# Optimization experiments

Measured on AMD Instinct MI355X. Metric: run time of the kernel, lower is better.

## Reference

```python
import jax, jax.numpy as jnp
import numpy as np

B, S, H = 64, 2048, 256
H3 = 3 * H


def setup_inputs() -> dict:
    key = jax.random.key(0)
    ks = jax.random.split(key, 5)
    static = jax.random.normal(ks[0], (B, S, H), dtype=jnp.float32)
    dynamic = jax.random.normal(ks[1], (B, S, H), dtype=jnp.float32)
    decoder_hidden = jax.random.normal(ks[2], (B, H), dtype=jnp.float32)
    # learned params (nn.Parameter in original); scale ~ 1/sqrt(fan_in)
    v = jax.random.normal(ks[3], (1, H3), dtype=jnp.float32) / np.sqrt(H3)
    W = jax.random.normal(ks[4], (H3, H3), dtype=jnp.float32) / np.sqrt(H3)
    return {"static": static, "dynamic": dynamic,
            "decoder_hidden": decoder_hidden, "v": v, "W": W}


def reference(static, dynamic, decoder_hidden, v, W):
    # cat = concat(static[i,j], dynamic[i,j], decoder_hidden[i]) -> [B, S, 3H]
    dec = jnp.broadcast_to(decoder_hidden[:, None, :], static.shape)
    cat = jnp.concatenate([static, dynamic, dec], axis=-1)
    # score[b,s] = v . tanh(W @ cat[b,s])
    hidden = jnp.tanh(jnp.einsum('ok,bsk->bso', W, cat))  # [B, S, 3H]
    scores = jnp.einsum('bso,o->bs', hidden, v[0])        # [B, S]
    return jax.nn.softmax(scores, axis=1)
```

## Files before the change

### kernel.cpp

```cpp
#include <hip/hip_runtime.h>
#include <hip/hip_bf16.h>

#define B_   64
#define S_   2048
#define H_   256
#define H3_  768
#define K_   512
#define MT   64

typedef __attribute__((ext_vector_type(8))) short  bf16x8;
typedef __attribute__((ext_vector_type(4))) float  f32x4;

__device__ __forceinline__ ushort f2bf(float f) {
    __hip_bfloat16 h = __float2bfloat16(f);
    return *reinterpret_cast<ushort*>(&h);
}

__device__ __forceinline__ float fast_tanh(float x) {
    float e = __expf(2.0f * x);
    return 1.0f - 2.0f / (e + 1.0f);
}

__global__ void pack_w(const float* __restrict__ W, short* __restrict__ wpk) {
    int t = blockIdx.x * 256 + threadIdx.x;
    if (t >= 48 * 16 * 64) return;
    int lane = t & 63;
    int ks   = (t >> 6) & 15;
    int ot   = t >> 10;
    int o  = ot * 16 + (lane & 15);
    int kb = ks * 32 + (lane >> 4) * 8;
    const float* src = W + (size_t)o * H3_ + kb;
    float4 a = ((const float4*)src)[0];
    float4 b = ((const float4*)src)[1];
    union { bf16x8 v; uint4 u; } pk;
    pk.u.x = (uint)f2bf(a.x) | ((uint)f2bf(a.y) << 16);
    pk.u.y = (uint)f2bf(a.z) | ((uint)f2bf(a.w) << 16);
    pk.u.z = (uint)f2bf(b.x) | ((uint)f2bf(b.y) << 16);
    pk.u.w = (uint)f2bf(b.z) | ((uint)f2bf(b.w) << 16);
    *(bf16x8*)(wpk + (size_t)t * 8) = pk.v;
}

__global__ void bias_k(const float* __restrict__ W, const float* __restrict__ dec,
                       float* __restrict__ bias) {
    int idx = blockIdx.x * 256 + threadIdx.x;
    if (idx >= B_ * H3_) return;
    int b = idx / H3_;
    int o = idx - b * H3_;
    const float4* wr = (const float4*)(W + (size_t)o * H3_ + 2 * H_);
    const float4* dv = (const float4*)(dec + (size_t)b * H_);
    float s = 0.f;
#pragma unroll 8
    for (int k = 0; k < H_ / 4; ++k) {
        float4 a = wr[k], d = dv[k];
        s += a.x * d.x + a.y * d.y + a.z * d.z + a.w * d.w;
    }
    bias[idx] = s;
}

__global__ __launch_bounds__(256, 2)
void score_k(const float* __restrict__ stat, const float* __restrict__ dyn,
             const short* __restrict__ wpk, const float* __restrict__ bias,
             const float* __restrict__ v, float* __restrict__ scores) {
    __shared__ short aT[MT * K_];
    __shared__ float sred[4][MT];

    const int tid  = threadIdx.x;
    const int pos0 = blockIdx.x * MT;
    const int bidx = pos0 >> 11;

#pragma unroll
    for (int bat = 0; bat < 2; ++bat) {
        float4 f0[8], f1[8];
#pragma unroll
        for (int u = 0; u < 8; ++u) {
            int lin = (bat * 8 + u) * 256 + tid;
            int row = lin >> 6;
            int k   = (lin & 63) * 8;
            const float* src = (k < 256)
                ? (stat + (size_t)(pos0 + row) * H_ + k)
                : (dyn  + (size_t)(pos0 + row) * H_ + (k - 256));
            f0[u] = ((const float4*)src)[0];
            f1[u] = ((const float4*)src)[1];
        }
#pragma unroll
        for (int u = 0; u < 8; ++u) {
            int lin = (bat * 8 + u) * 256 + tid;
            int row = lin >> 6;
            int k   = (lin & 63) * 8;
            uint4 pk;
            pk.x = (uint)f2bf(f0[u].x) | ((uint)f2bf(f0[u].y) << 16);
            pk.y = (uint)f2bf(f0[u].z) | ((uint)f2bf(f0[u].w) << 16);
            pk.z = (uint)f2bf(f1[u].x) | ((uint)f2bf(f1[u].y) << 16);
            pk.w = (uint)f2bf(f1[u].z) | ((uint)f2bf(f1[u].w) << 16);
            int off = row * (K_ * 2) + k * 2;
            off ^= (row & 7) << 4;
            *(uint4*)((char*)aT + off) = pk;
        }
    }
    __syncthreads();

    const int wave = tid >> 6;
    const int lane = tid & 63;
    const int lr = lane & 15;
    const int lg = lane >> 4;

    float sacc[4][4];
#pragma unroll
    for (int mi = 0; mi < 4; ++mi)
#pragma unroll
        for (int j = 0; j < 4; ++j) sacc[mi][j] = 0.f;

    for (int pass = 0; pass < 3; ++pass) {
        const int obase = pass * 256 + wave * 64;
        f32x4 acc[4][4];
#pragma unroll
        for (int mi = 0; mi < 4; ++mi)
#pragma unroll
            for (int ni = 0; ni < 4; ++ni) acc[mi][ni] = (f32x4)0.f;

#pragma unroll 4
        for (int ks = 0; ks < 16; ++ks) {
            bf16x8 bfr[4];
#pragma unroll
            for (int ni = 0; ni < 4; ++ni) {
                int ot = pass * 16 + wave * 4 + ni;
                bfr[ni] = *(const bf16x8*)(wpk +
                    ((size_t)(ot * 16 + ks) * 64 + lane) * 8);
            }
            const int kb = ks * 32 + lg * 8;
            bf16x8 afr[4];
#pragma unroll
            for (int mi = 0; mi < 4; ++mi) {
                int row = mi * 16 + lr;
                int off = row * (K_ * 2) + kb * 2;
                off ^= (row & 7) << 4;
                afr[mi] = *(const bf16x8*)((const char*)aT + off);
            }
#pragma unroll
            for (int mi = 0; mi < 4; ++mi)
#pragma unroll
                for (int ni = 0; ni < 4; ++ni)
                    acc[mi][ni] = __builtin_amdgcn_mfma_f32_16x16x32_bf16(
                        afr[mi], bfr[ni], acc[mi][ni], 0, 0, 0);
        }

#pragma unroll
        for (int ni = 0; ni < 4; ++ni) {
            int o = obase + ni * 16 + lr;
            float bv = bias[bidx * H3_ + o];
            float vv = v[o];
#pragma unroll
            for (int mi = 0; mi < 4; ++mi)
#pragma unroll
                for (int j = 0; j < 4; ++j)
                    sacc[mi][j] += vv * fast_tanh(acc[mi][ni][j] + bv);
        }
    }

#pragma unroll
    for (int mi = 0; mi < 4; ++mi)
#pragma unroll
        for (int j = 0; j < 4; ++j) {
            float x = sacc[mi][j];
            x += __shfl_xor(x, 1);
            x += __shfl_xor(x, 2);
            x += __shfl_xor(x, 4);
            x += __shfl_xor(x, 8);
            sacc[mi][j] = x;
        }
    if (lr == 0) {
#pragma unroll
        for (int mi = 0; mi < 4; ++mi)
#pragma unroll
            for (int j = 0; j < 4; ++j)
                sred[wave][mi * 16 + lg * 4 + j] = sacc[mi][j];
    }
    __syncthreads();
    if (tid < MT) {
        float s = sred[0][tid] + sred[1][tid] + sred[2][tid] + sred[3][tid];
        scores[pos0 + tid] = s;
    }
}

__global__ void softmax_k(float* __restrict__ out) {
    const int b = blockIdx.x;
    float* row = out + (size_t)b * S_;
    const int tid  = threadIdx.x;
    const int wave = tid >> 6;
    const int lane = tid & 63;

    float vals[8];
    float m = -1e30f;
#pragma unroll
    for (int i = 0; i < 8; ++i) {
        vals[i] = row[tid + i * 256];
        m = fmaxf(m, vals[i]);
    }
#pragma unroll
    for (int off = 32; off >= 1; off >>= 1) m = fmaxf(m, __shfl_xor(m, off));
    __shared__ float redm[4];
    __shared__ float reds[4];
    if (lane == 0) redm[wave] = m;
    __syncthreads();
    m = fmaxf(fmaxf(redm[0], redm[1]), fmaxf(redm[2], redm[3]));

    float s = 0.f;
#pragma unroll
    for (int i = 0; i < 8; ++i) {
        vals[i] = __expf(vals[i] - m);
        s += vals[i];
    }
#pragma unroll
    for (int off = 32; off >= 1; off >>= 1) s += __shfl_xor(s, off);
    if (lane == 0) reds[wave] = s;
    __syncthreads();
    s = reds[0] + reds[1] + reds[2] + reds[3];
    float inv = 1.0f / s;
#pragma unroll
    for (int i = 0; i < 8; ++i) row[tid + i * 256] = vals[i] * inv;
}

extern "C" void kernel_launch(void* const* d_in, const int* in_sizes, int n_in,
                              void* d_out, int out_size, void* d_ws, size_t ws_size,
                              hipStream_t stream) {
    const float* stat = (const float*)d_in[0];
    const float* dyn  = (const float*)d_in[1];
    const float* dec  = (const float*)d_in[2];
    const float* v    = (const float*)d_in[3];
    const float* W    = (const float*)d_in[4];
    float* out = (float*)d_out;

    short* wpk  = (short*)d_ws;
    float* bias = (float*)((char*)d_ws + (size_t)H3_ * K_ * 2);

    pack_w <<<(48 * 16 * 64 + 255) / 256, 256, 0, stream>>>(W, wpk);
    bias_k <<<(B_ * H3_ + 255) / 256, 256, 0, stream>>>(W, dec, bias);
    score_k<<<(B_ * S_) / MT, 256, 0, stream>>>(stat, dyn, wpk, bias, v, out);
    softmax_k<<<B_, 256, 0, stream>>>(out);
}
```

Before: 162.9 us.

## Double the row tile to 128 with 8 waves and pipeline K-chunk staging

The score kernel now handles 128 positions per block with 512 threads, and each wave owns a 96-column slice of the output so the W fragments are reused across 8 row tiles. The activation tile is staged in four K-quarters. The global loads for the next quarter are issued while MFMAs run on the current quarter, overlapping HBM latency with compute instead of loading everything up front. The trade-off is higher register pressure (8x3 accumulators plus prefetch buffers) and 128KB of LDS per block, which may limit occupancy to one block per CU.

```diff
diff --git a/kernel.cpp b/kernel.cpp
--- a/kernel.cpp
+++ b/kernel.cpp
@@ -6,7 +6,7 @@
 #define H_   256
 #define H3_  768
 #define K_   512
-#define MT   64
+#define MT   128
 
 typedef __attribute__((ext_vector_type(8))) short  bf16x8;
 typedef __attribute__((ext_vector_type(4))) float  f32x4;
@@ -57,46 +57,50 @@
     bias[idx] = s;
 }
 
-__global__ __launch_bounds__(256, 2)
+__global__ __launch_bounds__(512, 2)
 void score_k(const float* __restrict__ stat, const float* __restrict__ dyn,
              const short* __restrict__ wpk, const float* __restrict__ bias,
              const float* __restrict__ v, float* __restrict__ scores) {
-    __shared__ short aT[MT * K_];
-    __shared__ float sred[4][MT];
+    __shared__ short aT[4 * MT * 128];
+    __shared__ float sred[8][MT];
 
     const int tid  = threadIdx.x;
     const int pos0 = blockIdx.x * MT;
     const int bidx = pos0 >> 11;
 
-#pragma unroll
-    for (int bat = 0; bat < 2; ++bat) {
-        float4 f0[8], f1[8];
-#pragma unroll
-        for (int u = 0; u < 8; ++u) {
-            int lin = (bat * 8 + u) * 256 + tid;
-            int row = lin >> 6;
-            int k   = (lin & 63) * 8;
-            const float* src = (k < 256)
-                ? (stat + (size_t)(pos0 + row) * H_ + k)
-                : (dyn  + (size_t)(pos0 + row) * H_ + (k - 256));
+    float4 f0[4], f1[4];
+    auto stage_load = [&](int q) {
+#pragma unroll
+        for (int u = 0; u < 4; ++u) {
+            int lin = u * 512 + tid;
+            int row = lin >> 4;
+            int kl  = (lin & 15) * 8;
+            const float* src = (q < 2)
+                ? (stat + (size_t)(pos0 + row) * H_ + q * 128 + kl)
+                : (dyn  + (size_t)(pos0 + row) * H_ + (q - 2) * 128 + kl);
             f0[u] = ((const float4*)src)[0];
             f1[u] = ((const float4*)src)[1];
         }
-#pragma unroll
-        for (int u = 0; u < 8; ++u) {
-            int lin = (bat * 8 + u) * 256 + tid;
-            int row = lin >> 6;
-            int k   = (lin & 63) * 8;
+    };
+    auto stage_write = [&](int q) {
+#pragma unroll
+        for (int u = 0; u < 4; ++u) {
+            int lin = u * 512 + tid;
+            int row = lin >> 4;
+            int kl  = (lin & 15) * 8;
             uint4 pk;
             pk.x = (uint)f2bf(f0[u].x) | ((uint)f2bf(f0[u].y) << 16);
             pk.y = (uint)f2bf(f0[u].z) | ((uint)f2bf(f0[u].w) << 16);
             pk.z = (uint)f2bf(f1[u].x) | ((uint)f2bf(f1[u].y) << 16);
             pk.w = (uint)f2bf(f1[u].z) | ((uint)f2bf(f1[u].w) << 16);
-            int off = row * (K_ * 2) + k * 2;
+            int off = q * 32768 + row * 256 + kl * 2;
             off ^= (row & 7) << 4;
             *(uint4*)((char*)aT + off) = pk;
         }
-    }
+    };
+
+    stage_load(0);
+    stage_write(0);
     __syncthreads();
 
     const int wave = tid >> 6;
@@ -104,53 +108,58 @@
     const int lr = lane & 15;
     const int lg = lane >> 4;
 
-    float sacc[4][4];
-#pragma unroll
-    for (int mi = 0; mi < 4; ++mi)
+    float sacc[8][4];
+#pragma unroll
+    for (int mi = 0; mi < 8; ++mi)
 #pragma unroll
         for (int j = 0; j < 4; ++j) sacc[mi][j] = 0.f;
 
-    for (int pass = 0; pass < 3; ++pass) {
-        const int obase = pass * 256 + wave * 64;
-        f32x4 acc[4][4];
-#pragma unroll
-        for (int mi = 0; mi < 4; ++mi)
-#pragma unroll
-            for (int ni = 0; ni < 4; ++ni) acc[mi][ni] = (f32x4)0.f;
-
-#pragma unroll 4
-        for (int ks = 0; ks < 16; ++ks) {
-            bf16x8 bfr[4];
-#pragma unroll
-            for (int ni = 0; ni < 4; ++ni) {
-                int ot = pass * 16 + wave * 4 + ni;
-                bfr[ni] = *(const bf16x8*)(wpk +
-                    ((size_t)(ot * 16 + ks) * 64 + lane) * 8);
+    for (int p = 0; p < 2; ++p) {
+        f32x4 acc[8][3];
+#pragma unroll
+        for (int mi = 0; mi < 8; ++mi)
+#pragma unroll
+            for (int ni = 0; ni < 3; ++ni) acc[mi][ni] = (f32x4)0.f;
+
+#pragma unroll
+        for (int q = 0; q < 4; ++q) {
+            if (p == 0 && q < 3) stage_load(q + 1);
+#pragma unroll
+            for (int ksl = 0; ksl < 4; ++ksl) {
+                const int ks = q * 4 + ksl;
+                bf16x8 bfr[3];
+#pragma unroll
+                for (int ni = 0; ni < 3; ++ni) {
+                    int ot = wave * 6 + p * 3 + ni;
+                    bfr[ni] = *(const bf16x8*)(wpk +
+                        ((size_t)(ot * 16 + ks) * 64 + lane) * 8);
+                }
+                const int kbl = ksl * 32 + lg * 8;
+#pragma unroll
+                for (int mi = 0; mi < 8; ++mi) {
+                    int row = mi * 16 + lr;
+                    int off = q * 32768 + row * 256 + kbl * 2;
+                    off ^= (row & 7) << 4;
+                    bf16x8 afr = *(const bf16x8*)((const char*)aT + off);
+#pragma unroll
+                    for (int ni = 0; ni < 3; ++ni)
+                        acc[mi][ni] = __builtin_amdgcn_mfma_f32_16x16x32_bf16(
+                            afr, bfr[ni], acc[mi][ni], 0, 0, 0);
+                }
             }
-            const int kb = ks * 32 + lg * 8;
-            bf16x8 afr[4];
-#pragma unroll
-            for (int mi = 0; mi < 4; ++mi) {
-                int row = mi * 16 + lr;
-                int off = row * (K_ * 2) + kb * 2;
-                off ^= (row & 7) << 4;
-                afr[mi] = *(const bf16x8*)((const char*)aT + off);
+            if (p == 0 && q < 3) {
+                stage_write(q + 1);
+                __syncthreads();
             }
-#pragma unroll
-            for (int mi = 0; mi < 4; ++mi)
-#pragma unroll
-                for (int ni = 0; ni < 4; ++ni)
-                    acc[mi][ni] = __builtin_amdgcn_mfma_f32_16x16x32_bf16(
-                        afr[mi], bfr[ni], acc[mi][ni], 0, 0, 0);
-        }
-
-#pragma unroll
-        for (int ni = 0; ni < 4; ++ni) {
-            int o = obase + ni * 16 + lr;
+        }
+
+#pragma unroll
+        for (int ni = 0; ni < 3; ++ni) {
+            int o = wave * 96 + p * 48 + ni * 16 + lr;
             float bv = bias[bidx * H3_ + o];
             float vv = v[o];
 #pragma unroll
-            for (int mi = 0; mi < 4; ++mi)
+            for (int mi = 0; mi < 8; ++mi)
 #pragma unroll
                 for (int j = 0; j < 4; ++j)
                     sacc[mi][j] += vv * fast_tanh(acc[mi][ni][j] + bv);
@@ -158,7 +167,7 @@
     }
 
 #pragma unroll
-    for (int mi = 0; mi < 4; ++mi)
+    for (int mi = 0; mi < 8; ++mi)
 #pragma unroll
         for (int j = 0; j < 4; ++j) {
             float x = sacc[mi][j];
@@ -170,14 +179,16 @@
         }
     if (lr == 0) {
 #pragma unroll
-        for (int mi = 0; mi < 4; ++mi)
+        for (int mi = 0; mi < 8; ++mi)
 #pragma unroll
             for (int j = 0; j < 4; ++j)
                 sred[wave][mi * 16 + lg * 4 + j] = sacc[mi][j];
     }
     __syncthreads();
     if (tid < MT) {
-        float s = sred[0][tid] + sred[1][tid] + sred[2][tid] + sred[3][tid];
+        float s = 0.f;
+#pragma unroll
+        for (int w = 0; w < 8; ++w) s += sred[w][tid];
         scores[pos0 + tid] = s;
     }
 }
@@ -235,6 +246,6 @@
 
     pack_w <<<(48 * 16 * 64 + 255) / 256, 256, 0, stream>>>(W, wpk);
     bias_k <<<(B_ * H3_ + 255) / 256, 256, 0, stream>>>(W, dec, bias);
-    score_k<<<(B_ * S_) / MT, 256, 0, stream>>>(stat, dyn, wpk, bias, v, out);
+    score_k<<<(B_ * S_) / MT, 512, 0, stream>>>(stat, dyn, wpk, bias, v, out);
     softmax_k<<<B_, 256, 0, stream>>>(out);
 }
```

Result: slower. 525.2 us (+222.3%).

## Make score kernel persistent with register-prefetched next tile overlapping MFMA

Applied to the files above, without the earlier changes.

The score kernel now launches a fixed grid of 512 blocks, each processing four 64-row tiles. While the MFMA passes for the current tile run, global loads and bf16 conversion for the next tile are staged in registers and written to LDS after the current tile finishes. Each wave also now covers a contiguous 192-column output slice in four passes of three 16-column tiles, replacing three passes of four. This is meant to hide global-memory latency behind compute and cut block launch overhead, at the cost of much higher register pressure (16 packed uint4 plus prefetch buffers), which could hurt occupancy or cause spills under launch_bounds(256,2).

```diff
diff --git a/kernel.cpp b/kernel.cpp
--- a/kernel.cpp
+++ b/kernel.cpp
@@ -7,6 +7,7 @@
 #define H3_  768
 #define K_   512
 #define MT   64
+#define PBLK 512
 
 typedef __attribute__((ext_vector_type(8))) short  bf16x8;
 typedef __attribute__((ext_vector_type(4))) float  f32x4;
@@ -15,7 +16,9 @@
     __hip_bfloat16 h = __float2bfloat16(f);
     return *reinterpret_cast<ushort*>(&h);
 }
-
+__device__ __forceinline__ uint pkbf(float a, float b) {
+    return (uint)f2bf(a) | ((uint)f2bf(b) << 16);
+}
 __device__ __forceinline__ float fast_tanh(float x) {
     float e = __expf(2.0f * x);
     return 1.0f - 2.0f / (e + 1.0f);
@@ -33,10 +36,10 @@
     float4 a = ((const float4*)src)[0];
     float4 b = ((const float4*)src)[1];
     union { bf16x8 v; uint4 u; } pk;
-    pk.u.x = (uint)f2bf(a.x) | ((uint)f2bf(a.y) << 16);
-    pk.u.y = (uint)f2bf(a.z) | ((uint)f2bf(a.w) << 16);
-    pk.u.z = (uint)f2bf(b.x) | ((uint)f2bf(b.y) << 16);
-    pk.u.w = (uint)f2bf(b.z) | ((uint)f2bf(b.w) << 16);
+    pk.u.x = pkbf(a.x, a.y);
+    pk.u.y = pkbf(a.z, a.w);
+    pk.u.z = pkbf(b.x, b.y);
+    pk.u.w = pkbf(b.z, b.w);
     *(bf16x8*)(wpk + (size_t)t * 8) = pk.v;
 }
 
@@ -65,120 +68,146 @@
     __shared__ float sred[4][MT];
 
     const int tid  = threadIdx.x;
-    const int pos0 = blockIdx.x * MT;
-    const int bidx = pos0 >> 11;
-
-#pragma unroll
-    for (int bat = 0; bat < 2; ++bat) {
-        float4 f0[8], f1[8];
-#pragma unroll
-        for (int u = 0; u < 8; ++u) {
-            int lin = (bat * 8 + u) * 256 + tid;
-            int row = lin >> 6;
-            int k   = (lin & 63) * 8;
-            const float* src = (k < 256)
-                ? (stat + (size_t)(pos0 + row) * H_ + k)
-                : (dyn  + (size_t)(pos0 + row) * H_ + (k - 256));
-            f0[u] = ((const float4*)src)[0];
-            f1[u] = ((const float4*)src)[1];
-        }
-#pragma unroll
-        for (int u = 0; u < 8; ++u) {
-            int lin = (bat * 8 + u) * 256 + tid;
-            int row = lin >> 6;
-            int k   = (lin & 63) * 8;
-            uint4 pk;
-            pk.x = (uint)f2bf(f0[u].x) | ((uint)f2bf(f0[u].y) << 16);
-            pk.y = (uint)f2bf(f0[u].z) | ((uint)f2bf(f0[u].w) << 16);
-            pk.z = (uint)f2bf(f1[u].x) | ((uint)f2bf(f1[u].y) << 16);
-            pk.w = (uint)f2bf(f1[u].z) | ((uint)f2bf(f1[u].w) << 16);
-            int off = row * (K_ * 2) + k * 2;
-            off ^= (row & 7) << 4;
-            *(uint4*)((char*)aT + off) = pk;
-        }
-    }
-    __syncthreads();
-
     const int wave = tid >> 6;
     const int lane = tid & 63;
-    const int lr = lane & 15;
-    const int lg = lane >> 4;
-
-    float sacc[4][4];
-#pragma unroll
-    for (int mi = 0; mi < 4; ++mi)
-#pragma unroll
-        for (int j = 0; j < 4; ++j) sacc[mi][j] = 0.f;
-
-    for (int pass = 0; pass < 3; ++pass) {
-        const int obase = pass * 256 + wave * 64;
-        f32x4 acc[4][4];
+    const int lr   = lane & 15;
+    const int lg   = lane >> 4;
+
+    const int kcol = lane * 8;
+    const float* srcbase = (kcol < 256) ? (stat + kcol) : (dyn + (kcol - 256));
+
+    float4 f0[4], f1[4];
+    uint4  pk[16];
+
+    auto loadq = [&](int q, int gpos0) {
+#pragma unroll
+        for (int i = 0; i < 4; ++i) {
+            int u = q * 4 + i;
+            const float4* p = (const float4*)(srcbase + (size_t)(gpos0 + wave + u * 4) * H_);
+            f0[i] = p[0];
+            f1[i] = p[1];
+        }
+    };
+    auto cvtq = [&](int q) {
+#pragma unroll
+        for (int i = 0; i < 4; ++i) {
+            uint4 r;
+            r.x = pkbf(f0[i].x, f0[i].y);
+            r.y = pkbf(f0[i].z, f0[i].w);
+            r.z = pkbf(f1[i].x, f1[i].y);
+            r.w = pkbf(f1[i].z, f1[i].w);
+            pk[q * 4 + i] = r;
+        }
+    };
+    auto writeall = [&]() {
+#pragma unroll
+        for (int u = 0; u < 16; ++u) {
+            int row = wave + u * 4;
+            int off = ((row << 10) + (lane << 4)) ^ ((row & 7) << 4);
+            *(uint4*)((char*)aT + off) = pk[u];
+        }
+    };
+
+    {
+        const int g0 = blockIdx.x * MT;
+#pragma unroll
+        for (int q = 0; q < 4; ++q) { loadq(q, g0); cvtq(q); }
+        writeall();
+        __syncthreads();
+    }
+
+    const int swz = (lr & 7) << 4;
+
+#pragma unroll 1
+    for (int t = 0; t < 4; ++t) {
+        const int tile  = blockIdx.x + PBLK * t;
+        const int pos0  = tile * MT;
+        const int bidx  = pos0 >> 11;
+        const int pos0n = (blockIdx.x + PBLK * (t + 1)) * MT;
+
+        float sacc[4][4];
 #pragma unroll
         for (int mi = 0; mi < 4; ++mi)
 #pragma unroll
-            for (int ni = 0; ni < 4; ++ni) acc[mi][ni] = (f32x4)0.f;
+            for (int j = 0; j < 4; ++j) sacc[mi][j] = 0.f;
+
+#pragma unroll
+        for (int p = 0; p < 4; ++p) {
+            if (t < 3) {
+                if (p == 0)      { loadq(0, pos0n); }
+                else if (p == 1) { cvtq(0); loadq(1, pos0n); }
+                else if (p == 2) { cvtq(1); loadq(2, pos0n); }
+                else             { cvtq(2); loadq(3, pos0n); }
+            }
+
+            f32x4 acc[4][3];
+#pragma unroll
+            for (int mi = 0; mi < 4; ++mi)
+#pragma unroll
+                for (int ni = 0; ni < 3; ++ni) acc[mi][ni] = (f32x4)0.f;
+
+            const short* wp0 = wpk + ((size_t)((wave * 12 + p * 3) * 16) * 64 + lane) * 8;
 
 #pragma unroll 4
-        for (int ks = 0; ks < 16; ++ks) {
-            bf16x8 bfr[4];
-#pragma unroll
-            for (int ni = 0; ni < 4; ++ni) {
-                int ot = pass * 16 + wave * 4 + ni;
-                bfr[ni] = *(const bf16x8*)(wpk +
-                    ((size_t)(ot * 16 + ks) * 64 + lane) * 8);
-            }
-            const int kb = ks * 32 + lg * 8;
-            bf16x8 afr[4];
-#pragma unroll
-            for (int mi = 0; mi < 4; ++mi) {
-                int row = mi * 16 + lr;
-                int off = row * (K_ * 2) + kb * 2;
-                off ^= (row & 7) << 4;
-                afr[mi] = *(const bf16x8*)((const char*)aT + off);
-            }
+            for (int ks = 0; ks < 16; ++ks) {
+                bf16x8 bfr[3];
+#pragma unroll
+                for (int ni = 0; ni < 3; ++ni)
+                    bfr[ni] = *(const bf16x8*)(wp0 + ni * 8192 + ks * 512);
+                const int kb2 = ks * 64 + lg * 16;
+#pragma unroll
+                for (int mi = 0; mi < 4; ++mi) {
+                    int off = (((mi * 16 + lr) << 10) + kb2) ^ swz;
+                    bf16x8 afr = *(const bf16x8*)((const char*)aT + off);
+#pragma unroll
+                    for (int ni = 0; ni < 3; ++ni)
+                        acc[mi][ni] = __builtin_amdgcn_mfma_f32_16x16x32_bf16(
+                            afr, bfr[ni], acc[mi][ni], 0, 0, 0);
+                }
+            }
+
+#pragma unroll
+            for (int ni = 0; ni < 3; ++ni) {
+                int o = wave * 192 + p * 48 + ni * 16 + lr;
+                float bv = bias[bidx * H3_ + o];
+                float vv = v[o];
+#pragma unroll
+                for (int mi = 0; mi < 4; ++mi)
+#pragma unroll
+                    for (int j = 0; j < 4; ++j)
+                        sacc[mi][j] += vv * fast_tanh(acc[mi][ni][j] + bv);
+            }
+        }
+
+#pragma unroll
+        for (int mi = 0; mi < 4; ++mi)
+#pragma unroll
+            for (int j = 0; j < 4; ++j) {
+                float x = sacc[mi][j];
+                x += __shfl_xor(x, 1);
+                x += __shfl_xor(x, 2);
+                x += __shfl_xor(x, 4);
+                x += __shfl_xor(x, 8);
+                sacc[mi][j] = x;
+            }
+        if (lr == 0) {
 #pragma unroll
             for (int mi = 0; mi < 4; ++mi)
 #pragma unroll
-                for (int ni = 0; ni < 4; ++ni)
-                    acc[mi][ni] = __builtin_amdgcn_mfma_f32_16x16x32_bf16(
-                        afr[mi], bfr[ni], acc[mi][ni], 0, 0, 0);
-        }
-
-#pragma unroll
-        for (int ni = 0; ni < 4; ++ni) {
-            int o = obase + ni * 16 + lr;
-            float bv = bias[bidx * H3_ + o];
-            float vv = v[o];
-#pragma unroll
-            for (int mi = 0; mi < 4; ++mi)
-#pragma unroll
                 for (int j = 0; j < 4; ++j)
-                    sacc[mi][j] += vv * fast_tanh(acc[mi][ni][j] + bv);
-        }
-    }
-
-#pragma unroll
-    for (int mi = 0; mi < 4; ++mi)
-#pragma unroll
-        for (int j = 0; j < 4; ++j) {
-            float x = sacc[mi][j];
-            x += __shfl_xor(x, 1);
-            x += __shfl_xor(x, 2);
-            x += __shfl_xor(x, 4);
-            x += __shfl_xor(x, 8);
-            sacc[mi][j] = x;
-        }
-    if (lr == 0) {
-#pragma unroll
-        for (int mi = 0; mi < 4; ++mi)
-#pragma unroll
-            for (int j = 0; j < 4; ++j)
-                sred[wave][mi * 16 + lg * 4 + j] = sacc[mi][j];
-    }
-    __syncthreads();
-    if (tid < MT) {
-        float s = sred[0][tid] + sred[1][tid] + sred[2][tid] + sred[3][tid];
-        scores[pos0 + tid] = s;
+                    sred[wave][mi * 16 + lg * 4 + j] = sacc[mi][j];
+        }
+        __syncthreads();
+        if (tid < MT) {
+            float s = sred[0][tid] + sred[1][tid] + sred[2][tid] + sred[3][tid];
+            scores[pos0 + tid] = s;
+        }
+
+        if (t < 3) {
+            cvtq(3);
+            writeall();
+            __syncthreads();
+        }
     }
 }
 
@@ -235,6 +264,6 @@
 
     pack_w <<<(48 * 16 * 64 + 255) / 256, 256, 0, stream>>>(W, wpk);
     bias_k <<<(B_ * H3_ + 255) / 256, 256, 0, stream>>>(W, dec, bias);
-    score_k<<<(B_ * S_) / MT, 256, 0, stream>>>(stat, dyn, wpk, bias, v, out);
+    score_k<<<PBLK, 256, 0, stream>>>(stat, dyn, wpk, bias, v, out);
     softmax_k<<<B_, 256, 0, stream>>>(out);
 }
```

Result: slower. 302.7 us (+85.8%).
